# Performance work log

Hardware: AMD Instinct MI355X
Metric: run time of the kernel (lower is better)

The kernel has to match this reference:

```python
import jax, jax.numpy as jnp
import numpy as np

B, S, H, D = 4, 1024, 20, 64
DM = H * D          # 1280 model dim
DF = 4 * DM         # 5120 ffn dim
EPS = 1e-5          # haiku LayerNorm default


def setup_inputs() -> dict:
    key = jax.random.key(0)
    ks = jax.random.split(key, 12)
    sc = 1.0 / np.sqrt(DM)
    return {
        "x": jax.random.normal(ks[0], (B, S, DM), jnp.float32),
        "ln1_scale": jnp.ones((DM,), jnp.float32),
        "ln1_offset": jnp.zeros((DM,), jnp.float32),
        "wq": jax.random.normal(ks[1], (DM, DM), jnp.float32) * sc,
        "bq": jnp.zeros((DM,), jnp.float32),
        "wk": jax.random.normal(ks[2], (DM, DM), jnp.float32) * sc,
        "bk": jnp.zeros((DM,), jnp.float32),
        "wv": jax.random.normal(ks[3], (DM, DM), jnp.float32) * sc,
        "bv": jnp.zeros((DM,), jnp.float32),
        "wo": jax.random.normal(ks[4], (DM, DM), jnp.float32) * sc,
        "bo": jnp.zeros((DM,), jnp.float32),
        "ln2_scale": jnp.ones((DM,), jnp.float32),
        "ln2_offset": jnp.zeros((DM,), jnp.float32),
        "fc1_w": jax.random.normal(ks[5], (DM, DF), jnp.float32) * sc,
        "fc1_b": jnp.zeros((DF,), jnp.float32),
        "fc2_w": jax.random.normal(ks[6], (DF, DM), jnp.float32) * (1.0 / np.sqrt(DF)),
        "fc2_b": jnp.zeros((DM,), jnp.float32),
    }


def _layer_norm(x, scale, offset):
    m = jnp.mean(x, axis=-1, keepdims=True)
    v = jnp.mean(jnp.square(x - m), axis=-1, keepdims=True)
    return (x - m) * jax.lax.rsqrt(v + EPS) * scale + offset


def reference(x, ln1_scale, ln1_offset, wq, bq, wk, bk, wv, bv, wo, bo,
              ln2_scale, ln2_offset, fc1_w, fc1_b, fc2_w, fc2_b):
    b, s, dm = x.shape
    # --- self-attention sub-block ---
    res = x
    h = _layer_norm(x, ln1_scale, ln1_offset)
    q = (h @ wq + bq).reshape(b, s, H, D)
    k = (h @ wk + bk).reshape(b, s, H, D)
    v = (h @ wv + bv).reshape(b, s, H, D)
    logits = jnp.einsum('bthd,bThd->bhtT', q, k) / jnp.sqrt(jnp.asarray(D, x.dtype))
    weights = jax.nn.softmax(logits, axis=-1)
    attn = jnp.einsum('bhtT,bThd->bthd', weights, v).reshape(b, s, dm)
    x = res + (attn @ wo + bo)
    # --- MLP sub-block ---
    res = x
    h = _layer_norm(x, ln2_scale, ln2_offset)
    h = jax.nn.gelu(h @ fc1_w + fc1_b, approximate=False)
    x = res + (h @ fc2_w + fc2_b)
    return x
```

## Files before the change

kernel.cpp:

```cpp
#include <hip/hip_runtime.h>
#include <hip/hip_bf16.h>

typedef __hip_bfloat16 bf16;
typedef __attribute__((ext_vector_type(8))) short short8;
typedef __attribute__((ext_vector_type(4))) float f32x4;

#define DMODEL 1280
#define DFFN   5120
#define BATCH  4
#define SEQ    1024
#define NHEAD  20
#define HDIM   64
#define NROWS  (BATCH * SEQ)

#define GLDS(g, l) __builtin_amdgcn_global_load_lds(                            \
    (const __attribute__((address_space(1))) void*)(g),                         \
    (__attribute__((address_space(3))) void*)(l), 16, 0, 0)

__global__ __launch_bounds__(256) void transpose_cvt(
    const float* __restrict__ in, bf16* __restrict__ out, int K, int N)
{
    __shared__ float tile[32][33];
    const int n0 = blockIdx.x * 32;
    const int k0 = blockIdx.y * 32;
    const int tx = threadIdx.x;
    const int ty = threadIdx.y;
    for (int i = 0; i < 32; i += 8)
        tile[ty + i][tx] = in[(size_t)(k0 + ty + i) * N + (n0 + tx)];
    __syncthreads();
    for (int i = 0; i < 32; i += 8)
        out[(size_t)(n0 + ty + i) * K + (k0 + tx)] = __float2bfloat16(tile[tx][ty + i]);
}

__global__ __launch_bounds__(256) void transpose_cvt4(
    const float* __restrict__ s0, const float* __restrict__ s1,
    const float* __restrict__ s2, const float* __restrict__ s3,
    bf16* __restrict__ d0, bf16* __restrict__ d1,
    bf16* __restrict__ d2, bf16* __restrict__ d3)
{
    __shared__ float tile[32][33];
    const float* in;
    bf16* out;
    switch (blockIdx.z) {
        case 0: in = s0; out = d0; break;
        case 1: in = s1; out = d1; break;
        case 2: in = s2; out = d2; break;
        default: in = s3; out = d3; break;
    }
    const int n0 = blockIdx.x * 32;
    const int k0 = blockIdx.y * 32;
    const int tx = threadIdx.x;
    const int ty = threadIdx.y;
    for (int i = 0; i < 32; i += 8)
        tile[ty + i][tx] = in[(size_t)(k0 + ty + i) * DMODEL + (n0 + tx)];
    __syncthreads();
    for (int i = 0; i < 32; i += 8)
        out[(size_t)(n0 + ty + i) * DMODEL + (k0 + tx)] = __float2bfloat16(tile[tx][ty + i]);
}

__global__ __launch_bounds__(256) void pack_bias3(
    const float* __restrict__ a, const float* __restrict__ b,
    const float* __restrict__ c, float* __restrict__ o)
{
    const int i = blockIdx.x * 256 + threadIdx.x;
    if (i < DMODEL) {
        o[i] = a[i];
        o[DMODEL + i] = b[i];
        o[2 * DMODEL + i] = c[i];
    }
}

__global__ __launch_bounds__(256) void ln_bf16(
    const float* __restrict__ x, const float* __restrict__ sc,
    const float* __restrict__ of, bf16* __restrict__ out)
{
    const int row = blockIdx.x;
    const float* xr = x + (size_t)row * DMODEL;
    float v[5];
    float s = 0.f, s2 = 0.f;
    for (int i = 0; i < 5; ++i) {
        v[i] = xr[threadIdx.x + i * 256];
        s += v[i];
        s2 += v[i] * v[i];
    }
    for (int off = 1; off < 64; off <<= 1) {
        s  += __shfl_xor(s, off);
        s2 += __shfl_xor(s2, off);
    }
    __shared__ float red[2][4];
    const int wid = threadIdx.x >> 6;
    if ((threadIdx.x & 63) == 0) { red[0][wid] = s; red[1][wid] = s2; }
    __syncthreads();
    s  = red[0][0] + red[0][1] + red[0][2] + red[0][3];
    s2 = red[1][0] + red[1][1] + red[1][2] + red[1][3];
    const float mean = s * (1.0f / DMODEL);
    const float var  = s2 * (1.0f / DMODEL) - mean * mean;
    const float rstd = rsqrtf(var + 1e-5f);
    for (int i = 0; i < 5; ++i) {
        const int c = threadIdx.x + i * 256;
        const float y = (v[i] - mean) * rstd * sc[c] + of[c];
        out[(size_t)row * DMODEL + c] = __float2bfloat16(y);
    }
}

__global__ __launch_bounds__(256) void reduce2_ln(
    const float* __restrict__ P, const float* __restrict__ bias,
    const float* __restrict__ res, float* __restrict__ x1,
    const float* __restrict__ sc, const float* __restrict__ of,
    bf16* __restrict__ h2)
{
    const int row = blockIdx.x;
    const size_t base = (size_t)row * DMODEL;
    const int MN = NROWS * DMODEL;
    float v[5];
    float s = 0.f, s2 = 0.f;
    for (int i = 0; i < 5; ++i) {
        const int c = threadIdx.x + i * 256;
        const float val = P[base + c] + P[MN + base + c] + bias[c] + res[base + c];
        v[i] = val;
        x1[base + c] = val;
        s += val;
        s2 += val * val;
    }
    for (int off = 1; off < 64; off <<= 1) {
        s  += __shfl_xor(s, off);
        s2 += __shfl_xor(s2, off);
    }
    __shared__ float red[2][4];
    const int wid = threadIdx.x >> 6;
    if ((threadIdx.x & 63) == 0) { red[0][wid] = s; red[1][wid] = s2; }
    __syncthreads();
    s  = red[0][0] + red[0][1] + red[0][2] + red[0][3];
    s2 = red[1][0] + red[1][1] + red[1][2] + red[1][3];
    const float mean = s * (1.0f / DMODEL);
    const float var  = s2 * (1.0f / DMODEL) - mean * mean;
    const float rstd = rsqrtf(var + 1e-5f);
    for (int i = 0; i < 5; ++i) {
        const int c = threadIdx.x + i * 256;
        const float y = (v[i] - mean) * rstd * sc[c] + of[c];
        h2[base + c] = __float2bfloat16(y);
    }
}

template <int EPI>
__global__ __launch_bounds__(256) void gemm_bf16(
    const bf16* __restrict__ A, const bf16* __restrict__ Bt,
    const float* __restrict__ bias,
    bf16* __restrict__ Cb, float* __restrict__ Cf,
    int M, int N, int K, int klen)
{
    __shared__ bf16 As[128][32];
    __shared__ bf16 Bs[128][32];
    const int m0 = blockIdx.x * 128;
    const int n0 = blockIdx.y * 128;
    const int z  = blockIdx.z;
    const int kbeg = z * klen;
    const int kend = kbeg + klen;

    const int tid  = threadIdx.x;
    const int lane = tid & 63;
    const int wid  = tid >> 6;
    const int wm   = (wid >> 1) * 64;
    const int wn   = (wid & 1) * 64;
    const int l15  = lane & 15;
    const int lq   = lane >> 4;

    f32x4 acc[4][4];
    for (int i = 0; i < 4; ++i)
        for (int j = 0; j < 4; ++j)
            acc[i][j] = (f32x4){0.f, 0.f, 0.f, 0.f};

    const int sr  = tid >> 2;
    const int sc8 = (tid & 3) * 8;

    const bf16* aBase = A  + (size_t)(m0 + sr) * K + sc8;
    const bf16* bBase = Bt + (size_t)(n0 + sr) * K + sc8;

    for (int k0 = kbeg; k0 < kend; k0 += 32) {
        GLDS(aBase + k0,                  &As[sr][sc8]);
        GLDS(aBase + k0 + (size_t)64 * K, &As[64 + sr][sc8]);
        GLDS(bBase + k0,                  &Bs[sr][sc8]);
        GLDS(bBase + k0 + (size_t)64 * K, &Bs[64 + sr][sc8]);
        __syncthreads();

        short8 af[4], bfr[4];
        for (int mt = 0; mt < 4; ++mt)
            af[mt] = *(const short8*)(&As[wm + mt * 16 + l15][lq * 8]);
        for (int nt = 0; nt < 4; ++nt)
            bfr[nt] = *(const short8*)(&Bs[wn + nt * 16 + l15][lq * 8]);
        for (int mt = 0; mt < 4; ++mt)
            for (int nt = 0; nt < 4; ++nt)
                acc[mt][nt] = __builtin_amdgcn_mfma_f32_16x16x32_bf16(
                    af[mt], bfr[nt], acc[mt][nt], 0, 0, 0);
        __syncthreads();
    }

    float* Pf = Cf + (size_t)z * M * N;
    for (int mt = 0; mt < 4; ++mt)
        for (int nt = 0; nt < 4; ++nt)
            for (int r = 0; r < 4; ++r) {
                const int row = m0 + wm + mt * 16 + lq * 4 + r;
                const int col = n0 + wn + nt * 16 + l15;
                if (EPI == 0) {
                    const float v = acc[mt][nt][r] + bias[col];
                    Cb[(size_t)row * N + col] = __float2bfloat16(v);
                } else if (EPI == 2) {
                    const float v = acc[mt][nt][r] + bias[col];
                    const float g = 0.5f * v * (1.0f + erff(v * 0.70710678118654752f));
                    Cb[(size_t)row * N + col] = __float2bfloat16(g);
                } else {
                    Pf[(size_t)row * N + col] = acc[mt][nt][r];
                }
            }
}

__global__ __launch_bounds__(256) void reduce2(
    const float* __restrict__ P, const float* __restrict__ bias,
    const float* __restrict__ res, float* __restrict__ out, int MN, int N)
{
    const int i = (blockIdx.x * 256 + threadIdx.x) * 4;
    if (i >= MN) return;
    const float4 p0 = *(const float4*)(P + i);
    const float4 p1 = *(const float4*)(P + MN + i);
    const float4 r  = *(const float4*)(res + i);
    const float4 b  = *(const float4*)(bias + (i % N));
    float4 o;
    o.x = p0.x + p1.x + r.x + b.x;
    o.y = p0.y + p1.y + r.y + b.y;
    o.z = p0.z + p1.z + r.z + b.z;
    o.w = p0.w + p1.w + r.w + b.w;
    *(float4*)(out + i) = o;
}

__global__ __launch_bounds__(256) void flash_attn(
    const bf16* __restrict__ qb, const bf16* __restrict__ kb,
    const bf16* __restrict__ vb, bf16* __restrict__ ob, int ldq)
{
    __shared__ bf16 Ks[64][72];
    __shared__ bf16 Vt[64][72];
    __shared__ bf16 Ps[4][16][72];

    const int bh = blockIdx.y;
    const int b  = bh / NHEAD;
    const int hh = bh % NHEAD;
    const int q0 = blockIdx.x * 64;
    const int tid  = threadIdx.x;
    const int lane = tid & 63;
    const int wid  = tid >> 6;
    const int l15  = lane & 15;
    const int lq   = lane >> 4;

    short8 qf[2];
    {
        const bf16* qp = qb + ((size_t)(b * SEQ + q0 + wid * 16 + l15) * ldq)
                         + hh * HDIM + lq * 8;
        for (int kk = 0; kk < 2; ++kk) {
            union { short8 v; bf16 h[8]; } u;
            u.v = *(const short8*)(qp + kk * 32);
            for (int j = 0; j < 8; ++j)
                u.h[j] = __float2bfloat16(__bfloat162float(u.h[j]) * 0.125f);
            qf[kk] = u.v;
        }
    }

    float m_r[4] = {-INFINITY, -INFINITY, -INFINITY, -INFINITY};
    float l_r[4] = {0.f, 0.f, 0.f, 0.f};
    f32x4 o[4];
    for (int nt = 0; nt < 4; ++nt) o[nt] = (f32x4){0.f, 0.f, 0.f, 0.f};

    const int srow = tid >> 2;
    const int scol = (tid & 3) * 16;

    for (int j0 = 0; j0 < SEQ; j0 += 64) {
        const size_t gbase = (size_t)(b * SEQ + j0 + srow) * ldq + hh * HDIM + scol;
        uint4 kv0 = *(const uint4*)(kb + gbase);
        uint4 kv1 = *(const uint4*)(kb + gbase + 8);
        uint4 vv0 = *(const uint4*)(vb + gbase);
        uint4 vv1 = *(const uint4*)(vb + gbase + 8);
        __syncthreads();
        *(uint4*)(&Ks[srow][scol])     = kv0;
        *(uint4*)(&Ks[srow][scol + 8]) = kv1;
        {
            union { uint4 u[2]; bf16 h[16]; } tv;
            tv.u[0] = vv0; tv.u[1] = vv1;
            for (int i = 0; i < 16; ++i) Vt[scol + i][srow] = tv.h[i];
        }
        __syncthreads();

        f32x4 s[4];
        for (int nt = 0; nt < 4; ++nt) {
            f32x4 a = (f32x4){0.f, 0.f, 0.f, 0.f};
            for (int kk = 0; kk < 2; ++kk) {
                short8 kf = *(const short8*)(&Ks[nt * 16 + l15][lq * 8 + kk * 32]);
                a = __builtin_amdgcn_mfma_f32_16x16x32_bf16(qf[kk], kf, a, 0, 0, 0);
            }
            s[nt] = a;
        }

        for (int r = 0; r < 4; ++r) {
            float mx = fmaxf(fmaxf(s[0][r], s[1][r]), fmaxf(s[2][r], s[3][r]));
            for (int off = 1; off < 16; off <<= 1) mx = fmaxf(mx, __shfl_xor(mx, off));
            const float mnew  = fmaxf(m_r[r], mx);
            const float alpha = __expf(m_r[r] - mnew);
            float rs = 0.f;
            for (int nt = 0; nt < 4; ++nt) {
                const float p = __expf(s[nt][r] - mnew);
                s[nt][r] = p;
                rs += p;
            }
            for (int off = 1; off < 16; off <<= 1) rs += __shfl_xor(rs, off);
            l_r[r] = l_r[r] * alpha + rs;
            m_r[r] = mnew;
            for (int nt = 0; nt < 4; ++nt) o[nt][r] *= alpha;
        }

        for (int nt = 0; nt < 4; ++nt)
            for (int r = 0; r < 4; ++r)
                Ps[wid][lq * 4 + r][l15 + nt * 16] = __float2bfloat16(s[nt][r]);
        __syncthreads();

        for (int kk = 0; kk < 2; ++kk) {
            const short8 pf = *(const short8*)(&Ps[wid][l15][lq * 8 + kk * 32]);
            for (int nt = 0; nt < 4; ++nt) {
                const short8 vf = *(const short8*)(&Vt[l15 + nt * 16][lq * 8 + kk * 32]);
                o[nt] = __builtin_amdgcn_mfma_f32_16x16x32_bf16(pf, vf, o[nt], 0, 0, 0);
            }
        }
    }

    for (int r = 0; r < 4; ++r) {
        const float inv_l = 1.0f / l_r[r];
        const int row = q0 + wid * 16 + lq * 4 + r;
        for (int nt = 0; nt < 4; ++nt) {
            const int col = hh * HDIM + l15 + nt * 16;
            ob[(size_t)(b * SEQ + row) * DMODEL + col] =
                __float2bfloat16(o[nt][r] * inv_l);
        }
    }
}

extern "C" void kernel_launch(void* const* d_in, const int* in_sizes, int n_in,
                              void* d_out, int out_size, void* d_ws, size_t ws_size,
                              hipStream_t stream)
{
    (void)in_sizes; (void)n_in; (void)out_size; (void)ws_size;
    const float* x    = (const float*)d_in[0];
    const float* ln1s = (const float*)d_in[1];
    const float* ln1o = (const float*)d_in[2];
    const float* wq   = (const float*)d_in[3];
    const float* bq   = (const float*)d_in[4];
    const float* wk   = (const float*)d_in[5];
    const float* bk   = (const float*)d_in[6];
    const float* wv   = (const float*)d_in[7];
    const float* bv   = (const float*)d_in[8];
    const float* wo   = (const float*)d_in[9];
    const float* bo   = (const float*)d_in[10];
    const float* ln2s = (const float*)d_in[11];
    const float* ln2o = (const float*)d_in[12];
    const float* fc1w = (const float*)d_in[13];
    const float* fc1b = (const float*)d_in[14];
    const float* fc2w = (const float*)d_in[15];
    const float* fc2b = (const float*)d_in[16];
    float* out = (float*)d_out;

    char* wp = (char*)d_ws;
    auto alloc = [&](size_t n) { char* p = wp; wp += (n + 255) & ~(size_t)255; return p; };
    bf16*  wqkvt = (bf16*)alloc((size_t)3 * DMODEL * DMODEL * 2);
    bf16*  wot   = (bf16*)alloc((size_t)DMODEL * DMODEL * 2);
    bf16*  fc1t  = (bf16*)alloc((size_t)DFFN * DMODEL * 2);
    bf16*  fc2t  = (bf16*)alloc((size_t)DMODEL * DFFN * 2);
    float* bqkv  = (float*)alloc((size_t)3 * DMODEL * 4);
    char*  regA  = alloc((size_t)NROWS * DMODEL * 2
                       + (size_t)NROWS * 3 * DMODEL * 2
                       + (size_t)NROWS * DMODEL * 2);
    bf16*  h     = (bf16*)regA;
    bf16*  qkv   = (bf16*)(regA + (size_t)NROWS * DMODEL * 2);
    bf16*  attn  = (bf16*)(regA + (size_t)NROWS * 4 * DMODEL * 2);
    float* part  = (float*)regA;
    bf16*  h2    = (bf16*)alloc((size_t)NROWS * DMODEL * 2);
    bf16*  g     = (bf16*)alloc((size_t)NROWS * DFFN * 2);
    float* x1    = out;

    const dim3 tb(32, 8);
    transpose_cvt4<<<dim3(DMODEL / 32, DMODEL / 32, 4), tb, 0, stream>>>(
        wq, wk, wv, wo,
        wqkvt, wqkvt + (size_t)DMODEL * DMODEL, wqkvt + (size_t)2 * DMODEL * DMODEL, wot);
    transpose_cvt<<<dim3(DFFN / 32, DMODEL / 32), tb, 0, stream>>>(fc1w, fc1t, DMODEL, DFFN);
    transpose_cvt<<<dim3(DMODEL / 32, DFFN / 32), tb, 0, stream>>>(fc2w, fc2t, DFFN, DMODEL);
    pack_bias3<<<(DMODEL + 255) / 256, 256, 0, stream>>>(bq, bk, bv, bqkv);

    ln_bf16<<<NROWS, 256, 0, stream>>>(x, ln1s, ln1o, h);

    gemm_bf16<0><<<dim3(NROWS / 128, 3 * DMODEL / 128, 1), 256, 0, stream>>>(
        h, wqkvt, bqkv, qkv, nullptr, NROWS, 3 * DMODEL, DMODEL, DMODEL);

    flash_attn<<<dim3(SEQ / 64, BATCH * NHEAD), 256, 0, stream>>>(
        qkv, qkv + DMODEL, qkv + 2 * DMODEL, attn, 3 * DMODEL);

    gemm_bf16<3><<<dim3(NROWS / 128, DMODEL / 128, 2), 256, 0, stream>>>(
        attn, wot, nullptr, nullptr, part, NROWS, DMODEL, DMODEL, DMODEL / 2);
    reduce2_ln<<<NROWS, 256, 0, stream>>>(part, bo, x, x1, ln2s, ln2o, h2);

    gemm_bf16<2><<<dim3(NROWS / 128, DFFN / 128, 1), 256, 0, stream>>>(
        h2, fc1t, fc1b, g, nullptr, NROWS, DFFN, DMODEL, DMODEL);

    gemm_bf16<3><<<dim3(NROWS / 128, DMODEL / 128, 2), 256, 0, stream>>>(
        g, fc2t, nullptr, nullptr, part, NROWS, DMODEL, DFFN, DFFN / 2);
    reduce2<<<(NROWS * DMODEL / 4 + 255) / 256, 256, 0, stream>>>(
        part, fc2b, x1, out, NROWS * DMODEL, DMODEL);
}
```

Measured before the change: 560.3 us.

## Double-buffer GEMM LDS tiles with BK=64 and XOR-swizzled layout

The bf16 GEMM now keeps two LDS buffers of 128x64 for A and B. It prefetches the next K-tile with global_load_lds while MFMAs run on the current one, which removes one barrier per iteration. The K step grows from 32 to 64, and the columns are XOR-swizzled so the short8 fragment reads avoid LDS bank conflicts. LDS use rises to 64KB, which may limit occupancy, and klen must now be a multiple of 64.

```diff
diff --git a/kernel.cpp b/kernel.cpp
--- a/kernel.cpp
+++ b/kernel.cpp
@@ -149,13 +149,12 @@
     bf16* __restrict__ Cb, float* __restrict__ Cf,
     int M, int N, int K, int klen)
 {
-    __shared__ bf16 As[128][32];
-    __shared__ bf16 Bs[128][32];
+    __shared__ bf16 As[2][128][64];
+    __shared__ bf16 Bs[2][128][64];
     const int m0 = blockIdx.x * 128;
     const int n0 = blockIdx.y * 128;
     const int z  = blockIdx.z;
     const int kbeg = z * klen;
-    const int kend = kbeg + klen;
 
     const int tid  = threadIdx.x;
     const int lane = tid & 63;
@@ -164,35 +163,48 @@
     const int wn   = (wid & 1) * 64;
     const int l15  = lane & 15;
     const int lq   = lane >> 4;
+    const int l7   = l15 & 7;
 
     f32x4 acc[4][4];
     for (int i = 0; i < 4; ++i)
         for (int j = 0; j < 4; ++j)
             acc[i][j] = (f32x4){0.f, 0.f, 0.f, 0.f};
 
-    const int sr  = tid >> 2;
-    const int sc8 = (tid & 3) * 8;
-
-    const bf16* aBase = A  + (size_t)(m0 + sr) * K + sc8;
-    const bf16* bBase = Bt + (size_t)(n0 + sr) * K + sc8;
-
-    for (int k0 = kbeg; k0 < kend; k0 += 32) {
-        GLDS(aBase + k0,                  &As[sr][sc8]);
-        GLDS(aBase + k0 + (size_t)64 * K, &As[64 + sr][sc8]);
-        GLDS(bBase + k0,                  &Bs[sr][sc8]);
-        GLDS(bBase + k0 + (size_t)64 * K, &Bs[64 + sr][sc8]);
+    const int srow = lane >> 3;
+    const int cgl  = ((lane & 7) ^ srow) * 8;
+    const int lrow = wid * 8 + srow;
+    const int lcol = (lane & 7) * 8;
+
+    const bf16* aT = A  + (size_t)(m0 + lrow) * K + kbeg + cgl;
+    const bf16* bT = Bt + (size_t)(n0 + lrow) * K + kbeg + cgl;
+    const size_t rstep = (size_t)32 * K;
+
+    for (int i = 0; i < 4; ++i) GLDS(aT + i * rstep, &As[0][lrow + i * 32][lcol]);
+    for (int i = 0; i < 4; ++i) GLDS(bT + i * rstep, &Bs[0][lrow + i * 32][lcol]);
+
+    const int nIter = klen / 64;
+    for (int it = 0; it < nIter; ++it) {
+        const int buf = it & 1;
         __syncthreads();
-
-        short8 af[4], bfr[4];
-        for (int mt = 0; mt < 4; ++mt)
-            af[mt] = *(const short8*)(&As[wm + mt * 16 + l15][lq * 8]);
-        for (int nt = 0; nt < 4; ++nt)
-            bfr[nt] = *(const short8*)(&Bs[wn + nt * 16 + l15][lq * 8]);
-        for (int mt = 0; mt < 4; ++mt)
+        if (it + 1 < nIter) {
+            const int k1 = (it + 1) * 64;
+            for (int i = 0; i < 4; ++i)
+                GLDS(aT + k1 + i * rstep, &As[buf ^ 1][lrow + i * 32][lcol]);
+            for (int i = 0; i < 4; ++i)
+                GLDS(bT + k1 + i * rstep, &Bs[buf ^ 1][lrow + i * 32][lcol]);
+        }
+        for (int ko = 0; ko < 2; ++ko) {
+            const int ca = ((ko * 4 + lq) ^ l7) * 8;
+            short8 af[4], bfr[4];
+            for (int mt = 0; mt < 4; ++mt)
+                af[mt] = *(const short8*)(&As[buf][wm + mt * 16 + l15][ca]);
             for (int nt = 0; nt < 4; ++nt)
-                acc[mt][nt] = __builtin_amdgcn_mfma_f32_16x16x32_bf16(
-                    af[mt], bfr[nt], acc[mt][nt], 0, 0, 0);
-        __syncthreads();
+                bfr[nt] = *(const short8*)(&Bs[buf][wn + nt * 16 + l15][ca]);
+            for (int mt = 0; mt < 4; ++mt)
+                for (int nt = 0; nt < 4; ++nt)
+                    acc[mt][nt] = __builtin_amdgcn_mfma_f32_16x16x32_bf16(
+                        af[mt], bfr[nt], acc[mt][nt], 0, 0, 0);
+        }
     }
 
     float* Pf = Cf + (size_t)z * M * N;
```

After: 536.5 us. 4.2% less time.
